# Optimization experiments

Hardware: AMD Instinct MI355X
Metric: run time of the kernel (lower is better)

## Reference

```python
import jax, jax.numpy as jnp
import numpy as np

B, T, C = 8, 2048, 1024
HEAD = 64

def setup_inputs() -> dict:
    key = jax.random.key(0)
    k1, k2, k3, k4 = jax.random.split(key, 4)
    x = jax.random.normal(k1, (B, T, C), dtype=jnp.float32)
    # nn.Linear(n_embed, head_size, bias=False): y = x @ W^T; store as [C, HEAD] for x @ W
    scale = 1.0 / np.sqrt(C)
    Wq = jax.random.normal(k2, (C, HEAD), dtype=jnp.float32) * scale
    Wk = jax.random.normal(k3, (C, HEAD), dtype=jnp.float32) * scale
    Wv = jax.random.normal(k4, (C, HEAD), dtype=jnp.float32) * scale
    return {"x": x, "Wq": Wq, "Wk": Wk, "Wv": Wv}

def reference(x, Wq, Wk, Wv):
    Bx, Tx, Cx = x.shape
    q = x @ Wq            # [B,T,H]
    k = x @ Wk            # [B,T,H]
    v = x @ Wv            # [B,T,H]
    # NOTE: original scales by C**-0.5 (embedding dim), not head_size**-0.5
    aff = jnp.einsum('bqh,bkh->bqk', q, k) * (Cx ** -0.5)  # [B,T,T]
    causal = jnp.tril(jnp.ones((Tx, Tx), dtype=bool))
    aff = jnp.where(causal, aff, -jnp.inf)
    probs = jax.nn.softmax(aff, axis=-1)
    # dropout p=0.0 (eval): identity
    return jnp.einsum('bqk,bkh->bqh', probs, v)
```

## Files before the change

### kernel.cpp

```cpp
#include <hip/hip_runtime.h>
#include <hip/hip_bf16.h>

typedef __attribute__((ext_vector_type(8))) short bf16x8;
typedef __attribute__((ext_vector_type(4))) float f32x4;
typedef __attribute__((ext_vector_type(4))) int i32x4;

#define LOG2E 1.4426950408889634f

static __device__ __forceinline__ unsigned int f2bfu(float f) {
    return (unsigned int)__builtin_bit_cast(unsigned short, __float2bfloat16(f));
}
static __device__ __forceinline__ unsigned int pack2(float lo, float hi) {
    return (f2bfu(hi) << 16) | f2bfu(lo);
}
static __device__ __forceinline__ unsigned short f2bf(float f) {
    return __builtin_bit_cast(unsigned short, __float2bfloat16(f));
}

__global__ __launch_bounds__(256) void wtrans_kernel(
    const float* __restrict__ Wq, const float* __restrict__ Wk,
    const float* __restrict__ Wv, unsigned short* __restrict__ Wts)
{
    const int part = blockIdx.x;
    const int t    = blockIdx.y;
    const int c    = part * 256 + threadIdx.x;
    const int n    = c >> 3;
    const int mat  = n >> 6;
    const int nl   = n & 63;
    const int k0   = t * 64 + (c & 7) * 8;
    const float* W = (mat == 0) ? Wq : ((mat == 1) ? Wk : Wv);
    const float scale = (mat == 0) ? 0.03125f : 1.0f;
    unsigned int s[8];
#pragma unroll
    for (int j = 0; j < 8; ++j)
        s[j] = (unsigned int)f2bf(W[(size_t)(k0 + j) * 64 + nl] * scale);
    i32x4 pk;
    pk[0] = (int)(s[0] | (s[1] << 16));
    pk[1] = (int)(s[2] | (s[3] << 16));
    pk[2] = (int)(s[4] | (s[5] << 16));
    pk[3] = (int)(s[6] | (s[7] << 16));
    *(i32x4*)(Wts + (size_t)t * 12288 + (size_t)c * 8) = pk;
}

__global__ __launch_bounds__(256, 2) void proj_kernel(
    const float* __restrict__ x, const unsigned short* __restrict__ Wts,
    unsigned short* __restrict__ Qb, unsigned short* __restrict__ Kb,
    unsigned short* __restrict__ Vt)
{
    __shared__ __align__(16) unsigned short sA[2][32][72];
    __shared__ __align__(16) unsigned short sB[2][192][72];
    __shared__ __align__(16) unsigned short sVT[64][40];

    const int tid  = threadIdx.x;
    const int w    = tid >> 6;
    const int wm   = w >> 1;
    const int wn   = w & 1;
    const int lane = tid & 63;
    const int r    = lane & 15;
    const int g    = lane >> 4;
    const int mbase = blockIdx.x * 32;

    const int arow = tid >> 3;
    const int acb  = (tid & 7) * 8;
    const float* xptr = x + (size_t)(mbase + arow) * 1024 + acb;

    f32x4 acc[6];
#pragma unroll
    for (int i = 0; i < 6; ++i) acc[i] = (f32x4)0.0f;

    float4 XAa0, XAa1, XAb0, XAb1;
    i32x4 BB[6];

#define LOADX(S0, S1, t_) do { \
        const float* xp = xptr + (size_t)(t_) * 64; \
        S0 = *(const float4*)(xp);  S1 = *(const float4*)(xp + 4); \
    } while (0)

#define LOADB(t_) do { \
        const unsigned short* wp = Wts + (size_t)(t_) * 12288 + (size_t)tid * 8; \
        _Pragma("unroll") \
        for (int i = 0; i < 6; ++i) BB[i] = *(const i32x4*)(wp + i * 2048); \
    } while (0)

#define STORESTEP(buf, S0, S1) do { \
        i32x4 pa0 = {(int)pack2(S0.x, S0.y), (int)pack2(S0.z, S0.w), \
                     (int)pack2(S1.x, S1.y), (int)pack2(S1.z, S1.w)}; \
        *(i32x4*)&sA[buf][arow][acb] = pa0; \
        _Pragma("unroll") \
        for (int i = 0; i < 6; ++i) { \
            const int c = tid + 256 * i; \
            *(i32x4*)&sB[buf][c >> 3][(c & 7) * 8] = BB[i]; \
        } \
    } while (0)

#define COMPSTEP(buf) do { \
        _Pragma("unroll") \
        for (int h = 0; h < 2; ++h) { \
            bf16x8 af = *(const bf16x8*)&sA[buf][wm * 16 + r][h * 32 + g * 8]; \
            _Pragma("unroll") \
            for (int nt = 0; nt < 6; ++nt) { \
                bf16x8 bfr = *(const bf16x8*)&sB[buf][(nt * 2 + wn) * 16 + r][h * 32 + g * 8]; \
                acc[nt] = __builtin_amdgcn_mfma_f32_16x16x32_bf16(af, bfr, acc[nt], 0, 0, 0); \
            } \
        } \
    } while (0)

    LOADX(XAa0, XAa1, 0);
    LOADX(XAb0, XAb1, 1);
    LOADB(0);
#pragma unroll 1
    for (int t = 0; t < 16; t += 2) {
        STORESTEP(0, XAa0, XAa1);
        __syncthreads();
        if (t + 2 < 16) LOADX(XAa0, XAa1, t + 2);
        LOADB(t + 1);
        COMPSTEP(0);
        STORESTEP(1, XAb0, XAb1);
        __syncthreads();
        if (t + 3 < 16) LOADX(XAb0, XAb1, t + 3);
        if (t + 2 < 16) LOADB(t + 2);
        COMPSTEP(1);
    }

    const int row0 = mbase + wm * 16 + g * 4;
#pragma unroll
    for (int nt = 0; nt < 6; ++nt) {
        const int ti  = nt * 2 + wn;
        const int mat = ti >> 2;
        const int col = (ti & 3) * 16 + r;
#pragma unroll
        for (int j = 0; j < 4; ++j) {
            const float v = acc[nt][j];
            if (mat == 0) {
                Qb[(size_t)(row0 + j) * 64 + col] = f2bf(v);
            } else if (mat == 1) {
                Kb[(size_t)(row0 + j) * 64 + col] = f2bf(v);
            } else {
                sVT[col][wm * 16 + g * 4 + j] = f2bf(v);
            }
        }
    }
    __syncthreads();
    {
        const int h = tid >> 2, c = tid & 3;
        const int bb = mbase >> 11, tloc = mbase & 2047;
        unsigned short* dst = Vt + ((size_t)bb * 64 + h) * 2048 + tloc + c * 8;
        *(i32x4*)dst = *(const i32x4*)&sVT[h][c * 8];
    }
}

__global__ __launch_bounds__(512, 2) void attn_kernel(
    const unsigned short* __restrict__ Qb, const unsigned short* __restrict__ Kb,
    const unsigned short* __restrict__ Vt, float* __restrict__ out)
{
    __shared__ __align__(16) float sO[8][2][4][64][4];
    __shared__ float sM[8][2][16], sL[8][2][16];

    const int tid  = threadIdx.x;
    const int w    = tid >> 6;
    const int lane = tid & 63;
    const int r    = lane & 15;
    const int g    = lane >> 4;
    const int b    = blockIdx.x & 7;
    const int p    = blockIdx.x >> 3;
    const int qbL  = p * 32;
    const int qbH  = 2016 - p * 32;
    const int lastqL = qbL + 31;
    const int lastqH = qbH + 31;

    const unsigned short* Qbb = Qb + (size_t)b * 2048 * 64;
    const unsigned short* Kbb = Kb + (size_t)b * 2048 * 64;
    const unsigned short* Vtb = Vt + (size_t)b * 64 * 2048;

#define QBASE(qs) ((qs) < 2 ? (qbL + (qs) * 16) : (qbH + ((qs) - 2) * 16))

    bf16x8 qf[4][2];
#pragma unroll
    for (int qs = 0; qs < 4; ++qs)
#pragma unroll
        for (int h = 0; h < 2; ++h)
            qf[qs][h] = *(const bf16x8*)(Qbb + (size_t)(QBASE(qs) + r) * 64 + h * 32 + g * 8);

    f32x4 o[4][4];
#pragma unroll
    for (int qs = 0; qs < 4; ++qs)
#pragma unroll
        for (int i = 0; i < 4; ++i) o[qs][i] = (f32x4)0.0f;
    float m[4] = {-1e30f, -1e30f, -1e30f, -1e30f};
    float l[4] = {0.0f, 0.0f, 0.0f, 0.0f};

#define LOADK(K_, kv) do { \
        const int kra = (kv) + 8 * (r >> 2) + (r & 3); \
        K_[0] = *(const bf16x8*)(Kbb + (size_t)kra * 64 + g * 8); \
        K_[1] = *(const bf16x8*)(Kbb + (size_t)kra * 64 + 32 + g * 8); \
        K_[2] = *(const bf16x8*)(Kbb + (size_t)(kra + 4) * 64 + g * 8); \
        K_[3] = *(const bf16x8*)(Kbb + (size_t)(kra + 4) * 64 + 32 + g * 8); \
    } while (0)
#define LOADV(V_, kv) do { _Pragma("unroll") \
        for (int i = 0; i < 4; ++i) \
            V_[i] = *(const bf16x8*)(Vtb + (size_t)(i * 16 + r) * 2048 + (kv) + g * 8); \
    } while (0)

    bf16x8 KA[4], VA[4];
#pragma unroll 1
    for (int kv0 = w * 32; kv0 <= lastqH; kv0 += 256) {
        const bool doLow = (kv0 <= lastqL);

        LOADK(KA, kv0);
        LOADV(VA, kv0);

        f32x4 s0[4], s1[4];
        __builtin_amdgcn_s_setprio(1);
#pragma unroll
        for (int qs = 0; qs < 4; ++qs) {
            s0[qs] = (f32x4)0.0f; s1[qs] = (f32x4)0.0f;
            if (qs < 2 && !doLow) continue;
            s0[qs] = __builtin_amdgcn_mfma_f32_16x16x32_bf16(KA[0], qf[qs][0], s0[qs], 0, 0, 0);
            s0[qs] = __builtin_amdgcn_mfma_f32_16x16x32_bf16(KA[1], qf[qs][1], s0[qs], 0, 0, 0);
            s1[qs] = __builtin_amdgcn_mfma_f32_16x16x32_bf16(KA[2], qf[qs][0], s1[qs], 0, 0, 0);
            s1[qs] = __builtin_amdgcn_mfma_f32_16x16x32_bf16(KA[3], qf[qs][1], s1[qs], 0, 0, 0);
        }
        __builtin_amdgcn_s_setprio(0);

        float lm[4] = {-1e30f, -1e30f, -1e30f, -1e30f};
#pragma unroll
        for (int qs = 0; qs < 4; ++qs) {
            if (qs < 2 && !doLow) continue;
            const int q = QBASE(qs) + r;
            if (kv0 + 31 > QBASE(qs)) {
#pragma unroll
                for (int j = 0; j < 4; ++j) {
                    if (kv0 + 8 * g + j > q)     s0[qs][j] = -1e30f;
                    if (kv0 + 8 * g + 4 + j > q) s1[qs][j] = -1e30f;
                }
            }
            lm[qs] = fmaxf(fmaxf(fmaxf(s0[qs][0], s0[qs][1]), fmaxf(s0[qs][2], s0[qs][3])),
                           fmaxf(fmaxf(s1[qs][0], s1[qs][1]), fmaxf(s1[qs][2], s1[qs][3])));
        }
        if (!__all(lm[0] <= m[0] + 8.0f && lm[1] <= m[1] + 8.0f &&
                   lm[2] <= m[2] + 8.0f && lm[3] <= m[3] + 8.0f)) {
#pragma unroll
            for (int qs = 0; qs < 4; ++qs) {
                float t2 = fmaxf(lm[qs], __shfl_xor(lm[qs], 16));
                t2 = fmaxf(t2, __shfl_xor(t2, 32));
                const float mn = fmaxf(m[qs], t2);
                const float alpha = __builtin_amdgcn_exp2f((m[qs] - mn) * LOG2E);
#pragma unroll
                for (int ht = 0; ht < 4; ++ht) o[qs][ht] *= alpha;
                l[qs] *= alpha;
                m[qs] = mn;
            }
        }

        __builtin_amdgcn_s_setprio(1);
#pragma unroll
        for (int qs = 0; qs < 4; ++qs) {
            if (qs < 2 && !doLow) continue;
            float p0[4], p1[4];
#pragma unroll
            for (int j = 0; j < 4; ++j) {
                p0[j] = __builtin_amdgcn_exp2f((s0[qs][j] - m[qs]) * LOG2E);
                p1[j] = __builtin_amdgcn_exp2f((s1[qs][j] - m[qs]) * LOG2E);
                l[qs] += p0[j] + p1[j];
            }
            i32x4 pw;
            pw[0] = (int)pack2(p0[0], p0[1]);
            pw[1] = (int)pack2(p0[2], p0[3]);
            pw[2] = (int)pack2(p1[0], p1[1]);
            pw[3] = (int)pack2(p1[2], p1[3]);
            bf16x8 pfrag = __builtin_bit_cast(bf16x8, pw);
            o[qs][0] = __builtin_amdgcn_mfma_f32_16x16x32_bf16(VA[0], pfrag, o[qs][0], 0, 0, 0);
            o[qs][1] = __builtin_amdgcn_mfma_f32_16x16x32_bf16(VA[1], pfrag, o[qs][1], 0, 0, 0);
            o[qs][2] = __builtin_amdgcn_mfma_f32_16x16x32_bf16(VA[2], pfrag, o[qs][2], 0, 0, 0);
            o[qs][3] = __builtin_amdgcn_mfma_f32_16x16x32_bf16(VA[3], pfrag, o[qs][3], 0, 0, 0);
        }
        __builtin_amdgcn_s_setprio(0);
    }

#define MERGE_STORE(QS, Q2) do { \
        float lr = l[QS]; \
        lr += __shfl_xor(lr, 16); \
        lr += __shfl_xor(lr, 32); \
        if (g == 0) { sM[w][Q2][r] = m[QS]; sL[w][Q2][r] = lr; } \
        _Pragma("unroll") \
        for (int ht = 0; ht < 4; ++ht) *(f32x4*)&sO[w][Q2][ht][lane][0] = o[QS][ht]; \
    } while (0)

#define MERGE_WRITE(QBASE0) do { \
        const int q2 = w >> 2, ht = w & 3; \
        float M = sM[0][q2][r]; \
        _Pragma("unroll") \
        for (int wp = 1; wp < 8; ++wp) M = fmaxf(M, sM[wp][q2][r]); \
        float L = 0.0f; \
        float beta[8]; \
        _Pragma("unroll") \
        for (int wp = 0; wp < 8; ++wp) { \
            beta[wp] = __builtin_amdgcn_exp2f((sM[wp][q2][r] - M) * LOG2E); \
            L += beta[wp] * sL[wp][q2][r]; \
        } \
        f32x4 av = (f32x4)0.0f; \
        _Pragma("unroll") \
        for (int wp = 0; wp < 8; ++wp) { \
            f32x4 t = *(const f32x4*)&sO[wp][q2][ht][lane][0]; \
            av += t * beta[wp]; \
        } \
        const float inv = 1.0f / L; \
        const int qrow = (QBASE0) + q2 * 16 + r; \
        *(f32x4*)(out + ((size_t)b * 2048 + qrow) * 64 + ht * 16 + g * 4) = av * inv; \
    } while (0)

    MERGE_STORE(0, 0);
    MERGE_STORE(1, 1);
    __syncthreads();
    MERGE_WRITE(qbL);
    __syncthreads();
    MERGE_STORE(2, 0);
    MERGE_STORE(3, 1);
    __syncthreads();
    MERGE_WRITE(qbH);
}

extern "C" void kernel_launch(void* const* d_in, const int* in_sizes, int n_in,
                              void* d_out, int out_size, void* d_ws, size_t ws_size,
                              hipStream_t stream) {
    const float* x  = (const float*)d_in[0];
    const float* Wq = (const float*)d_in[1];
    const float* Wk = (const float*)d_in[2];
    const float* Wv = (const float*)d_in[3];
    float* out = (float*)d_out;

    unsigned short* Qb  = (unsigned short*)d_ws;
    unsigned short* Kb  = Qb + (size_t)8 * 2048 * 64;
    unsigned short* Vt  = Kb + (size_t)8 * 2048 * 64;
    unsigned short* Wts = Vt + (size_t)8 * 64 * 2048;

    hipLaunchKernelGGL(wtrans_kernel, dim3(6, 16), dim3(256), 0, stream, Wq, Wk, Wv, Wts);
    hipLaunchKernelGGL(proj_kernel, dim3(512), dim3(256), 0, stream, x, Wts, Qb, Kb, Vt);
    hipLaunchKernelGGL(attn_kernel, dim3(256), dim3(512), 0, stream, Qb, Kb, Vt, out);
}
```

Baseline: 47.91 us.

## Deepen x prefetch in projection and double-buffer K loads in attention

The projection GEMM loop now holds four x tiles in registers instead of two, prefetching x four steps ahead. The attention loop is unrolled by two, with two K register buffers so the next K block loads while the current block computes. V for each block is loaded just before its compute. Both changes aim to hide global memory latency behind MFMA work, at the cost of more registers and possible occupancy loss.

```diff
diff --git a/kernel.cpp b/kernel.cpp
--- a/kernel.cpp
+++ b/kernel.cpp
@@ -68,7 +68,7 @@
 #pragma unroll
     for (int i = 0; i < 6; ++i) acc[i] = (f32x4)0.0f;
 
-    float4 XAa0, XAa1, XAb0, XAb1;
+    float4 XAa0, XAa1, XAb0, XAb1, XAc0, XAc1, XAd0, XAd1;
     i32x4 BB[6];
 
 #define LOADX(S0, S1, t_) do { \
@@ -107,18 +107,33 @@
 
     LOADX(XAa0, XAa1, 0);
     LOADX(XAb0, XAb1, 1);
+    LOADX(XAc0, XAc1, 2);
+    LOADX(XAd0, XAd1, 3);
     LOADB(0);
 #pragma unroll 1
-    for (int t = 0; t < 16; t += 2) {
+    for (int t = 0; t < 16; t += 4) {
         STORESTEP(0, XAa0, XAa1);
         __syncthreads();
-        if (t + 2 < 16) LOADX(XAa0, XAa1, t + 2);
+        if (t + 4 < 16) LOADX(XAa0, XAa1, t + 4);
         LOADB(t + 1);
         COMPSTEP(0);
+
         STORESTEP(1, XAb0, XAb1);
         __syncthreads();
-        if (t + 3 < 16) LOADX(XAb0, XAb1, t + 3);
-        if (t + 2 < 16) LOADB(t + 2);
+        if (t + 5 < 16) LOADX(XAb0, XAb1, t + 5);
+        LOADB(t + 2);
+        COMPSTEP(1);
+
+        STORESTEP(0, XAc0, XAc1);
+        __syncthreads();
+        if (t + 6 < 16) LOADX(XAc0, XAc1, t + 6);
+        LOADB(t + 3);
+        COMPSTEP(0);
+
+        STORESTEP(1, XAd0, XAd1);
+        __syncthreads();
+        if (t + 7 < 16) LOADX(XAd0, XAd1, t + 7);
+        if (t + 4 < 16) LOADB(t + 4);
         COMPSTEP(1);
     }
 
@@ -201,80 +216,88 @@
             V_[i] = *(const bf16x8*)(Vtb + (size_t)(i * 16 + r) * 2048 + (kv) + g * 8); \
     } while (0)
 
-    bf16x8 KA[4], VA[4];
+#define COMPUTE(K_, V_, kv0v) do { \
+    const bool doLow = ((kv0v) <= lastqL); \
+    f32x4 s0[4], s1[4]; \
+    __builtin_amdgcn_s_setprio(1); \
+    _Pragma("unroll") \
+    for (int qs = 0; qs < 4; ++qs) { \
+        s0[qs] = (f32x4)0.0f; s1[qs] = (f32x4)0.0f; \
+        if (qs < 2 && !doLow) continue; \
+        s0[qs] = __builtin_amdgcn_mfma_f32_16x16x32_bf16(K_[0], qf[qs][0], s0[qs], 0, 0, 0); \
+        s0[qs] = __builtin_amdgcn_mfma_f32_16x16x32_bf16(K_[1], qf[qs][1], s0[qs], 0, 0, 0); \
+        s1[qs] = __builtin_amdgcn_mfma_f32_16x16x32_bf16(K_[2], qf[qs][0], s1[qs], 0, 0, 0); \
+        s1[qs] = __builtin_amdgcn_mfma_f32_16x16x32_bf16(K_[3], qf[qs][1], s1[qs], 0, 0, 0); \
+    } \
+    __builtin_amdgcn_s_setprio(0); \
+    float lm[4] = {-1e30f, -1e30f, -1e30f, -1e30f}; \
+    _Pragma("unroll") \
+    for (int qs = 0; qs < 4; ++qs) { \
+        if (qs < 2 && !doLow) continue; \
+        const int q = QBASE(qs) + r; \
+        if ((kv0v) + 31 > QBASE(qs)) { \
+            _Pragma("unroll") \
+            for (int j = 0; j < 4; ++j) { \
+                if ((kv0v) + 8 * g + j > q)     s0[qs][j] = -1e30f; \
+                if ((kv0v) + 8 * g + 4 + j > q) s1[qs][j] = -1e30f; \
+            } \
+        } \
+        lm[qs] = fmaxf(fmaxf(fmaxf(s0[qs][0], s0[qs][1]), fmaxf(s0[qs][2], s0[qs][3])), \
+                       fmaxf(fmaxf(s1[qs][0], s1[qs][1]), fmaxf(s1[qs][2], s1[qs][3]))); \
+    } \
+    if (!__all(lm[0] <= m[0] + 8.0f && lm[1] <= m[1] + 8.0f && \
+               lm[2] <= m[2] + 8.0f && lm[3] <= m[3] + 8.0f)) { \
+        _Pragma("unroll") \
+        for (int qs = 0; qs < 4; ++qs) { \
+            float t2 = fmaxf(lm[qs], __shfl_xor(lm[qs], 16)); \
+            t2 = fmaxf(t2, __shfl_xor(t2, 32)); \
+            const float mn = fmaxf(m[qs], t2); \
+            const float alpha = __builtin_amdgcn_exp2f((m[qs] - mn) * LOG2E); \
+            _Pragma("unroll") \
+            for (int ht = 0; ht < 4; ++ht) o[qs][ht] *= alpha; \
+            l[qs] *= alpha; \
+            m[qs] = mn; \
+        } \
+    } \
+    __builtin_amdgcn_s_setprio(1); \
+    _Pragma("unroll") \
+    for (int qs = 0; qs < 4; ++qs) { \
+        if (qs < 2 && !doLow) continue; \
+        float p0[4], p1[4]; \
+        _Pragma("unroll") \
+        for (int j = 0; j < 4; ++j) { \
+            p0[j] = __builtin_amdgcn_exp2f((s0[qs][j] - m[qs]) * LOG2E); \
+            p1[j] = __builtin_amdgcn_exp2f((s1[qs][j] - m[qs]) * LOG2E); \
+            l[qs] += p0[j] + p1[j]; \
+        } \
+        i32x4 pw; \
+        pw[0] = (int)pack2(p0[0], p0[1]); \
+        pw[1] = (int)pack2(p0[2], p0[3]); \
+        pw[2] = (int)pack2(p1[0], p1[1]); \
+        pw[3] = (int)pack2(p1[2], p1[3]); \
+        bf16x8 pfrag = __builtin_bit_cast(bf16x8, pw); \
+        o[qs][0] = __builtin_amdgcn_mfma_f32_16x16x32_bf16(V_[0], pfrag, o[qs][0], 0, 0, 0); \
+        o[qs][1] = __builtin_amdgcn_mfma_f32_16x16x32_bf16(V_[1], pfrag, o[qs][1], 0, 0, 0); \
+        o[qs][2] = __builtin_amdgcn_mfma_f32_16x16x32_bf16(V_[2], pfrag, o[qs][2], 0, 0, 0); \
+        o[qs][3] = __builtin_amdgcn_mfma_f32_16x16x32_bf16(V_[3], pfrag, o[qs][3], 0, 0, 0); \
+    } \
+    __builtin_amdgcn_s_setprio(0); \
+    } while (0)
+
+    bf16x8 K0[4], K1[4], VA[4];
+    LOADK(K0, w * 32);
 #pragma unroll 1
-    for (int kv0 = w * 32; kv0 <= lastqH; kv0 += 256) {
-        const bool doLow = (kv0 <= lastqL);
-
-        LOADK(KA, kv0);
+    for (int kv0 = w * 32; kv0 <= lastqH; kv0 += 512) {
+        const int kvB = kv0 + 256;
         LOADV(VA, kv0);
-
-        f32x4 s0[4], s1[4];
-        __builtin_amdgcn_s_setprio(1);
-#pragma unroll
-        for (int qs = 0; qs < 4; ++qs) {
-            s0[qs] = (f32x4)0.0f; s1[qs] = (f32x4)0.0f;
-            if (qs < 2 && !doLow) continue;
-            s0[qs] = __builtin_amdgcn_mfma_f32_16x16x32_bf16(KA[0], qf[qs][0], s0[qs], 0, 0, 0);
-            s0[qs] = __builtin_amdgcn_mfma_f32_16x16x32_bf16(KA[1], qf[qs][1], s0[qs], 0, 0, 0);
-            s1[qs] = __builtin_amdgcn_mfma_f32_16x16x32_bf16(KA[2], qf[qs][0], s1[qs], 0, 0, 0);
-            s1[qs] = __builtin_amdgcn_mfma_f32_16x16x32_bf16(KA[3], qf[qs][1], s1[qs], 0, 0, 0);
+        if (kvB <= lastqH) LOADK(K1, kvB);
+        COMPUTE(K0, VA, kv0);
+        if (kvB <= lastqH) {
+            const int kvC = kv0 + 512;
+            LOADV(VA, kvB);
+            if (kvC <= lastqH) LOADK(K0, kvC);
+            COMPUTE(K1, VA, kvB);
         }
-        __builtin_amdgcn_s_setprio(0);
-
-        float lm[4] = {-1e30f, -1e30f, -1e30f, -1e30f};
-#pragma unroll
-        for (int qs = 0; qs < 4; ++qs) {
-            if (qs < 2 && !doLow) continue;
-            const int q = QBASE(qs) + r;
-            if (kv0 + 31 > QBASE(qs)) {
-#pragma unroll
-                for (int j = 0; j < 4; ++j) {
-                    if (kv0 + 8 * g + j > q)     s0[qs][j] = -1e30f;
-                    if (kv0 + 8 * g + 4 + j > q) s1[qs][j] = -1e30f;
-                }
-            }
-            lm[qs] = fmaxf(fmaxf(fmaxf(s0[qs][0], s0[qs][1]), fmaxf(s0[qs][2], s0[qs][3])),
-                           fmaxf(fmaxf(s1[qs][0], s1[qs][1]), fmaxf(s1[qs][2], s1[qs][3])));
-        }
-        if (!__all(lm[0] <= m[0] + 8.0f && lm[1] <= m[1] + 8.0f &&
-                   lm[2] <= m[2] + 8.0f && lm[3] <= m[3] + 8.0f)) {
-#pragma unroll
-            for (int qs = 0; qs < 4; ++qs) {
-                float t2 = fmaxf(lm[qs], __shfl_xor(lm[qs], 16));
-                t2 = fmaxf(t2, __shfl_xor(t2, 32));
-                const float mn = fmaxf(m[qs], t2);
-                const float alpha = __builtin_amdgcn_exp2f((m[qs] - mn) * LOG2E);
-#pragma unroll
-                for (int ht = 0; ht < 4; ++ht) o[qs][ht] *= alpha;
-                l[qs] *= alpha;
-                m[qs] = mn;
-            }
-        }
-
-        __builtin_amdgcn_s_setprio(1);
-#pragma unroll
-        for (int qs = 0; qs < 4; ++qs) {
-            if (qs < 2 && !doLow) continue;
-            float p0[4], p1[4];
-#pragma unroll
-            for (int j = 0; j < 4; ++j) {
-                p0[j] = __builtin_amdgcn_exp2f((s0[qs][j] - m[qs]) * LOG2E);
-                p1[j] = __builtin_amdgcn_exp2f((s1[qs][j] - m[qs]) * LOG2E);
-                l[qs] += p0[j] + p1[j];
-            }
-            i32x4 pw;
-            pw[0] = (int)pack2(p0[0], p0[1]);
-            pw[1] = (int)pack2(p0[2], p0[3]);
-            pw[2] = (int)pack2(p1[0], p1[1]);
-            pw[3] = (int)pack2(p1[2], p1[3]);
-            bf16x8 pfrag = __builtin_bit_cast(bf16x8, pw);
-            o[qs][0] = __builtin_amdgcn_mfma_f32_16x16x32_bf16(VA[0], pfrag, o[qs][0], 0, 0, 0);
-            o[qs][1] = __builtin_amdgcn_mfma_f32_16x16x32_bf16(VA[1], pfrag, o[qs][1], 0, 0, 0);
-            o[qs][2] = __builtin_amdgcn_mfma_f32_16x16x32_bf16(VA[2], pfrag, o[qs][2], 0, 0, 0);
-            o[qs][3] = __builtin_amdgcn_mfma_f32_16x16x32_bf16(VA[3], pfrag, o[qs][3], 0, 0, 0);
-        }
-        __builtin_amdgcn_s_setprio(0);
     }
 
 #define MERGE_STORE(QS, Q2) do { \
```

Result: slower. 49.80 us (+4.0%).

## Store K and V in pre-swizzled MFMA fragment layout for coalesced attention loads

Applied to the files above, without the earlier changes.

The projection kernel now stages K through shared memory and writes K and V tiles in the exact per-lane fragment order the attention kernel's MFMA uses. Each 32-key tile becomes four contiguous 512-element blocks. The attention kernel can then load each fragment with a fully contiguous 16-byte-per-lane read instead of strided row gathers. This adds an extra shared-memory buffer and store pass in the projection kernel.

```diff
diff --git a/kernel.cpp b/kernel.cpp
--- a/kernel.cpp
+++ b/kernel.cpp
@@ -44,12 +44,13 @@
 
 __global__ __launch_bounds__(256, 2) void proj_kernel(
     const float* __restrict__ x, const unsigned short* __restrict__ Wts,
-    unsigned short* __restrict__ Qb, unsigned short* __restrict__ Kb,
-    unsigned short* __restrict__ Vt)
+    unsigned short* __restrict__ Qb, unsigned short* __restrict__ Kp,
+    unsigned short* __restrict__ Vp)
 {
     __shared__ __align__(16) unsigned short sA[2][32][72];
     __shared__ __align__(16) unsigned short sB[2][192][72];
-    __shared__ __align__(16) unsigned short sVT[64][40];
+    __shared__ __align__(16) unsigned short sVT[64][48];
+    __shared__ __align__(16) unsigned short sK[32][72];
 
     const int tid  = threadIdx.x;
     const int w    = tid >> 6;
@@ -122,7 +123,8 @@
         COMPSTEP(1);
     }
 
-    const int row0 = mbase + wm * 16 + g * 4;
+    const int row0  = mbase + wm * 16 + g * 4;
+    const int lrow0 = wm * 16 + g * 4;
 #pragma unroll
     for (int nt = 0; nt < 6; ++nt) {
         const int ti  = nt * 2 + wn;
@@ -134,24 +136,30 @@
             if (mat == 0) {
                 Qb[(size_t)(row0 + j) * 64 + col] = f2bf(v);
             } else if (mat == 1) {
-                Kb[(size_t)(row0 + j) * 64 + col] = f2bf(v);
+                sK[lrow0 + j][col] = f2bf(v);
             } else {
-                sVT[col][wm * 16 + g * 4 + j] = f2bf(v);
+                sVT[col][lrow0 + j] = f2bf(v);
             }
         }
     }
     __syncthreads();
     {
-        const int h = tid >> 2, c = tid & 3;
-        const int bb = mbase >> 11, tloc = mbase & 2047;
-        unsigned short* dst = Vt + ((size_t)bb * 64 + h) * 2048 + tloc + c * 8;
-        *(i32x4*)dst = *(const i32x4*)&sVT[h][c * 8];
+        const int bb = mbase >> 11;
+        const int t  = (mbase & 2047) >> 5;
+        const int f  = tid >> 6;
+        const int r2 = lane & 15, g2 = lane >> 4;
+        const int krow = 8 * (r2 >> 2) + (r2 & 3) + (f >> 1) * 4;
+        const int kcol = (f & 1) * 32 + g2 * 8;
+        *(i32x4*)(Kp + ((size_t)(bb * 64 + t) * 4 + f) * 512 + lane * 8)
+            = *(const i32x4*)&sK[krow][kcol];
+        *(i32x4*)(Vp + ((size_t)(bb * 64 + t) * 4 + f) * 512 + lane * 8)
+            = *(const i32x4*)&sVT[f * 16 + r2][g2 * 8];
     }
 }
 
 __global__ __launch_bounds__(512, 2) void attn_kernel(
-    const unsigned short* __restrict__ Qb, const unsigned short* __restrict__ Kb,
-    const unsigned short* __restrict__ Vt, float* __restrict__ out)
+    const unsigned short* __restrict__ Qb, const unsigned short* __restrict__ Kp,
+    const unsigned short* __restrict__ Vp, float* __restrict__ out)
 {
     __shared__ __align__(16) float sO[8][2][4][64][4];
     __shared__ float sM[8][2][16], sL[8][2][16];
@@ -169,8 +177,8 @@
     const int lastqH = qbH + 31;
 
     const unsigned short* Qbb = Qb + (size_t)b * 2048 * 64;
-    const unsigned short* Kbb = Kb + (size_t)b * 2048 * 64;
-    const unsigned short* Vtb = Vt + (size_t)b * 64 * 2048;
+    const unsigned short* Kpb = Kp + (size_t)b * 64 * 2048;
+    const unsigned short* Vpb = Vp + (size_t)b * 64 * 2048;
 
 #define QBASE(qs) ((qs) < 2 ? (qbL + (qs) * 16) : (qbH + ((qs) - 2) * 16))
 
@@ -189,16 +197,17 @@
     float m[4] = {-1e30f, -1e30f, -1e30f, -1e30f};
     float l[4] = {0.0f, 0.0f, 0.0f, 0.0f};
 
-#define LOADK(K_, kv) do { \
-        const int kra = (kv) + 8 * (r >> 2) + (r & 3); \
-        K_[0] = *(const bf16x8*)(Kbb + (size_t)kra * 64 + g * 8); \
-        K_[1] = *(const bf16x8*)(Kbb + (size_t)kra * 64 + 32 + g * 8); \
-        K_[2] = *(const bf16x8*)(Kbb + (size_t)(kra + 4) * 64 + g * 8); \
-        K_[3] = *(const bf16x8*)(Kbb + (size_t)(kra + 4) * 64 + 32 + g * 8); \
-    } while (0)
-#define LOADV(V_, kv) do { _Pragma("unroll") \
-        for (int i = 0; i < 4; ++i) \
-            V_[i] = *(const bf16x8*)(Vtb + (size_t)(i * 16 + r) * 2048 + (kv) + g * 8); \
+#define LOADK(K_, kvt) do { \
+        const unsigned short* kp = Kpb + (size_t)(kvt) * 2048 + lane * 8; \
+        K_[0] = *(const bf16x8*)(kp); \
+        K_[1] = *(const bf16x8*)(kp + 512); \
+        K_[2] = *(const bf16x8*)(kp + 1024); \
+        K_[3] = *(const bf16x8*)(kp + 1536); \
+    } while (0)
+#define LOADV(V_, kvt) do { \
+        const unsigned short* vp = Vpb + (size_t)(kvt) * 2048 + lane * 8; \
+        _Pragma("unroll") \
+        for (int i = 0; i < 4; ++i) V_[i] = *(const bf16x8*)(vp + i * 512); \
     } while (0)
 
     bf16x8 KA[4], VA[4];
@@ -206,8 +215,8 @@
     for (int kv0 = w * 32; kv0 <= lastqH; kv0 += 256) {
         const bool doLow = (kv0 <= lastqL);
 
-        LOADK(KA, kv0);
-        LOADV(VA, kv0);
+        LOADK(KA, kv0 >> 5);
+        LOADV(VA, kv0 >> 5);
 
         f32x4 s0[4], s1[4];
         __builtin_amdgcn_s_setprio(1);
@@ -330,11 +339,11 @@
     float* out = (float*)d_out;
 
     unsigned short* Qb  = (unsigned short*)d_ws;
-    unsigned short* Kb  = Qb + (size_t)8 * 2048 * 64;
-    unsigned short* Vt  = Kb + (size_t)8 * 2048 * 64;
-    unsigned short* Wts = Vt + (size_t)8 * 64 * 2048;
+    unsigned short* Kp  = Qb + (size_t)8 * 2048 * 64;
+    unsigned short* Vp  = Kp + (size_t)8 * 64 * 2048;
+    unsigned short* Wts = Vp + (size_t)8 * 64 * 2048;
 
     hipLaunchKernelGGL(wtrans_kernel, dim3(6, 16), dim3(256), 0, stream, Wq, Wk, Wv, Wts);
-    hipLaunchKernelGGL(proj_kernel, dim3(512), dim3(256), 0, stream, x, Wts, Qb, Kb, Vt);
-    hipLaunchKernelGGL(attn_kernel, dim3(256), dim3(512), 0, stream, Qb, Kb, Vt, out);
-}
+    hipLaunchKernelGGL(proj_kernel, dim3(512), dim3(256), 0, stream, x, Wts, Qb, Kp, Vp);
+    hipLaunchKernelGGL(attn_kernel, dim3(256), dim3(512), 0, stream, Qb, Kp, Vp, out);
+}
```

Measured after the change: 41.44 us. -13.5%, faster.
